# Kernel optimization log

Hardware: AMD Instinct MI355X
Metric: run time of the kernel (lower is better)

The kernel has to match this reference:

```python
import jax, jax.numpy as jnp
import numpy as np

H = 16        # attention heads
KVH = 4       # kv heads (GQA)
D = 128       # qk head_dim = qk_nope(64) + qk_rope(64)
ROPE = 64     # rotary sub-dim
VCH = 128     # v_channels
HID = 2048    # hidden size
E = 8         # routed experts
K = 2         # top-k
EPS = 1e-6
THETA = 10000.0


def rmsnorm(x, w):
    return x * jax.lax.rsqrt(jnp.mean(x * x, axis=-1, keepdims=True) + EPS) * w


def apply_rope(x, pos):
    # x: [T, h, ROPE]; rotate-half convention on the rope sub-dim
    half = ROPE // 2
    inv_freq = 1.0 / (THETA ** (jnp.arange(half, dtype=jnp.float32) / half))
    ang = pos.astype(jnp.float32)[:, None] * inv_freq          # [T, half]
    cos = jnp.cos(ang)[:, None, :]
    sin = jnp.sin(ang)[:, None, :]
    x1, x2 = x[..., :half], x[..., half:]
    return jnp.concatenate([x1 * cos - x2 * sin, x1 * sin + x2 * cos], axis=-1)


def swiglu(x, w_gate, w_up, w_down):
    return (jax.nn.silu(x @ w_gate) * (x @ w_up)) @ w_down


def setup_inputs() -> dict:
    key = jax.random.key(0)
    ks = jax.random.split(key, 16)
    T = 2048
    sc = 0.02
    n = lambda k, s: jax.random.normal(k, s, dtype=jnp.float32) * sc
    return {
        "x": jax.random.normal(ks[0], (T, HID), dtype=jnp.float32),
        "positions": jnp.arange(T, dtype=jnp.int32),
        "ln1_w": jnp.ones((HID,), jnp.float32),
        "qkv_w": n(ks[1], (HID, H * D + KVH * D + KVH * VCH)),
        "qkv_b": n(ks[2], (H * D + KVH * D + KVH * VCH,)),
        "k_ln_w": jnp.ones((D,), jnp.float32),
        "o_w": n(ks[3], (H * VCH, HID)),
        "ln2_w": jnp.ones((HID,), jnp.float32),
        "router_w": n(ks[4], (HID, E)),
        "w1": n(ks[5], (E, HID, 512)),
        "w2": n(ks[6], (E, 512, HID)),
        "w3": n(ks[7], (E, HID, 512)),
        "sw1": n(ks[8], (HID, 1024)),
        "sw2": n(ks[9], (1024, HID)),
        "sw3": n(ks[10], (HID, 1024)),
    }


def reference(x, positions, ln1_w, qkv_w, qkv_b, k_ln_w, o_w, ln2_w,
              router_w, w1, w2, w3, sw1, sw2, sw3):
    T = x.shape[0]
    # --- attention block ---
    h = rmsnorm(x, ln1_w)
    qkv = h @ qkv_w + qkv_b
    q = qkv[:, : H * D].reshape(T, H, D)
    k = qkv[:, H * D : H * D + KVH * D].reshape(T, KVH, D)
    v = qkv[:, H * D + KVH * D :].reshape(T, KVH, VCH)
    k = rmsnorm(k, k_ln_w)  # per-head k_layernorm over head_dim
    # rope applied to the trailing qk_rope_dim of q/k
    q = jnp.concatenate([q[..., : D - ROPE], apply_rope(q[..., D - ROPE :], positions)], -1)
    k = jnp.concatenate([k[..., : D - ROPE], apply_rope(k[..., D - ROPE :], positions)], -1)
    rep = H // KVH
    kf = jnp.repeat(k, rep, axis=1)   # [T, H, D]
    vf = jnp.repeat(v, rep, axis=1)   # [T, H, VCH]
    scale = D ** -0.5
    scores = jnp.einsum("qhd,khd->hqk", q, kf) * scale
    causal = jnp.tril(jnp.ones((T, T), dtype=bool))
    scores = jnp.where(causal[None], scores, jnp.float32(-1e30))
    p = jax.nn.softmax(scores, axis=-1)
    attn = jnp.einsum("hqk,khv->qhv", p, vf).reshape(T, H * VCH)
    x = x + attn @ o_w
    # --- MoE block: shared expert + top-k routed experts ---
    h2 = rmsnorm(x, ln2_w)
    probs = jax.nn.softmax(h2 @ router_w, axis=-1)            # [T, E]
    topw, topi = jax.lax.top_k(probs, K)
    topw = topw / jnp.sum(topw, axis=-1, keepdims=True)        # renormalize top-k
    combine = jnp.sum(jax.nn.one_hot(topi, E, dtype=h2.dtype) * topw[..., None], axis=1)  # [T, E]
    moe = swiglu(h2, sw1, sw3, sw2)                            # shared expert
    for e in range(E):  # small fixed expert count
        moe = moe + combine[:, e : e + 1] * swiglu(h2, w1[e], w3[e], w2[e])
    return x + moe
```

## Files before the change

### kernel.cpp

```cpp
#include <hip/hip_runtime.h>


typedef _Float16 half_t;
typedef _Float16 half8 __attribute__((ext_vector_type(8)));
typedef float    f32x4 __attribute__((ext_vector_type(4)));
typedef float    floatx4 __attribute__((ext_vector_type(4)));

#define T_TOK 2048
#define HIDN  2048
#define NH    16
#define NKVH  4
#define HD    128
#define QKV_N 3072
#define NEXP  8
#define NPAIR_MAX 4608

#define MFMA16(a,b,c) __builtin_amdgcn_mfma_f32_16x16x32_f16(a,b,c,0,0,0)

__device__ __forceinline__ void gload_lds16(const half_t* g, half_t* l) {
    __builtin_amdgcn_global_load_lds(
        (const __attribute__((address_space(1))) void*)g,
        (__attribute__((address_space(3))) void*)l, 16, 0, 0);
}

__device__ __forceinline__ float silu_f(float g) {
    return g / (1.0f + expf(-g));
}

__global__ __launch_bounds__(256)
void rmsnorm_split_k(const float* __restrict__ x, const float* __restrict__ w,
                     half_t* __restrict__ hi, half_t* __restrict__ lo)
{
    const int row = blockIdx.x, tid = threadIdx.x;
    const float* xr = x + (size_t)row * HIDN;
    floatx4 v0 = *(const floatx4*)(xr + tid * 8);
    floatx4 v1 = *(const floatx4*)(xr + tid * 8 + 4);
    float ss = v0[0]*v0[0] + v0[1]*v0[1] + v0[2]*v0[2] + v0[3]*v0[3]
             + v1[0]*v1[0] + v1[1]*v1[1] + v1[2]*v1[2] + v1[3]*v1[3];
    for (int o = 32; o; o >>= 1) ss += __shfl_down(ss, o);
    __shared__ float red[4];
    if ((tid & 63) == 0) red[tid >> 6] = ss;
    __syncthreads();
    ss = red[0] + red[1] + red[2] + red[3];
    float rs = rsqrtf(ss * (1.0f / HIDN) + 1e-6f);
    floatx4 w0 = *(const floatx4*)(w + tid * 8);
    floatx4 w1 = *(const floatx4*)(w + tid * 8 + 4);
    float vv[8] = { v0[0]*w0[0], v0[1]*w0[1], v0[2]*w0[2], v0[3]*w0[3],
                    v1[0]*w1[0], v1[1]*w1[1], v1[2]*w1[2], v1[3]*w1[3] };
    half8 hv, lv;
#pragma unroll
    for (int j = 0; j < 8; ++j) {
        float o = vv[j] * rs;
        half_t h = (half_t)o;
        hv[j] = h;
        lv[j] = (half_t)((o - (float)h) * 1024.0f);
    }
    *(half8*)(hi + (size_t)row * HIDN + tid * 8) = hv;
    if (lo) *(half8*)(lo + (size_t)row * HIDN + tid * 8) = lv;
}

__global__ __launch_bounds__(256)
void transpose_split2(const float* __restrict__ src,
                      half_t* __restrict__ dh, half_t* __restrict__ dl,
                      int sstride, int dstride)
{
    __shared__ float tile[32][36];
    const int n0 = blockIdx.x * 32, k0 = blockIdx.y * 32;
    const int tid = threadIdx.x;
    {
        int r = tid >> 3, c = (tid & 7) * 4;
        *(floatx4*)&tile[r][c] =
            *(const floatx4*)(src + (size_t)(k0 + r) * sstride + n0 + c);
    }
    __syncthreads();
    int n = tid & 31, g = tid >> 5, gg = g & 3;
    half8 hv;
    if (g < 4) {
#pragma unroll
        for (int j = 0; j < 8; ++j) hv[j] = (half_t)tile[gg * 8 + j][n];
        *(half8*)(dh + (size_t)(n0 + n) * dstride + k0 + gg * 8) = hv;
    } else {
#pragma unroll
        for (int j = 0; j < 8; ++j) {
            float v = tile[gg * 8 + j][n];
            half_t h = (half_t)v;
            hv[j] = (half_t)((v - (float)h) * 1024.0f);
        }
        *(half8*)(dl + (size_t)(n0 + n) * dstride + k0 + gg * 8) = hv;
    }
}

__global__ __launch_bounds__(256)
void transpose_f16(const float* __restrict__ src, half_t* __restrict__ dh,
                   int sstride, int dstride)
{
    __shared__ float tile[32][68];
    const int n0 = blockIdx.x * 64, k0 = blockIdx.y * 32;
    const int tid = threadIdx.x;
    {
        int r = tid >> 3, c = (tid & 7) * 4;
        const float* s = src + (size_t)(k0 + r) * sstride + n0;
        *(floatx4*)&tile[r][c]      = *(const floatx4*)(s + c);
        *(floatx4*)&tile[r][c + 32] = *(const floatx4*)(s + c + 32);
    }
    __syncthreads();
    int n = tid & 63, g = tid >> 6;
    half8 hv;
#pragma unroll
    for (int j = 0; j < 8; ++j) hv[j] = (half_t)tile[g * 8 + j][n];
    *(half8*)(dh + (size_t)(n0 + n) * dstride + k0 + g * 8) = hv;
}

__global__ __launch_bounds__(256)
void w13_transpose(const float* __restrict__ sw1, const float* __restrict__ w1,
                   const float* __restrict__ sw3, const float* __restrict__ w3,
                   half_t* __restrict__ dst)
{
    __shared__ float tile[32][68];
    const int n0 = blockIdx.x * 64, k0 = blockIdx.y * 32;
    const int tid = threadIdx.x;
    const float* base;
    int stride;
    if (n0 < 1024)      { base = sw1 + n0; stride = 1024; }
    else if (n0 < 2048) { base = sw3 + (n0 - 1024); stride = 1024; }
    else if (n0 < 6144) { int e = (n0 - 2048) >> 9;
                          base = w1 + (size_t)e * HIDN * 512 + ((n0 - 2048) & 511);
                          stride = 512; }
    else                { int e = (n0 - 6144) >> 9;
                          base = w3 + (size_t)e * HIDN * 512 + ((n0 - 6144) & 511);
                          stride = 512; }
    {
        int r = tid >> 3, c = (tid & 7) * 4;
        const float* s = base + (size_t)(k0 + r) * stride;
        *(floatx4*)&tile[r][c]      = *(const floatx4*)(s + c);
        *(floatx4*)&tile[r][c + 32] = *(const floatx4*)(s + c + 32);
    }
    __syncthreads();
    int n = tid & 63, g = tid >> 6;
    half8 hv;
#pragma unroll
    for (int j = 0; j < 8; ++j) hv[j] = (half_t)tile[g * 8 + j][n];
    *(half8*)(dst + (size_t)(n0 + n) * HIDN + k0 + g * 8) = hv;
}

__global__ __launch_bounds__(256)
void w2_transpose(const float* __restrict__ sw2, const float* __restrict__ w2,
                  half_t* __restrict__ dst)
{
    __shared__ float tile[32][68];
    const int n0 = blockIdx.x * 64, k0 = blockIdx.y * 32;
    const int tid = threadIdx.x;
    {
        int r = tid >> 3, c = (tid & 7) * 4;
        int k = k0 + r;
        const float* s;
        if (k < 1024) s = sw2 + (size_t)k * HIDN + n0;
        else {
            int e = (k - 1024) >> 9, kk = (k - 1024) & 511;
            s = w2 + ((size_t)e * 512 + kk) * HIDN + n0;
        }
        *(floatx4*)&tile[r][c]      = *(const floatx4*)(s + c);
        *(floatx4*)&tile[r][c + 32] = *(const floatx4*)(s + c + 32);
    }
    __syncthreads();
    int n = tid & 63, g = tid >> 6;
    half8 hv;
#pragma unroll
    for (int j = 0; j < 8; ++j) hv[j] = (half_t)tile[g * 8 + j][n];
    *(half8*)(dst + (size_t)(n0 + n) * 5120 + k0 + g * 8) = hv;
}

__global__ __launch_bounds__(256)
void owu_kernel(const float* __restrict__ ow, const float* __restrict__ ln2w,
                const float* __restrict__ rw, float* __restrict__ owu,
                int* __restrict__ cnt, int* __restrict__ pairTok,
                float* __restrict__ pairW)
{
    if (blockIdx.x < 18) {
        int idx = blockIdx.x * 256 + threadIdx.x;
        if (idx < NPAIR_MAX) { pairTok[idx] = 0; pairW[idx] = 0.0f; }
        if (idx < NEXP) cnt[idx] = 0;
    }
    const int k = blockIdx.x * 4 + (threadIdx.x >> 6);
    const int lane = threadIdx.x & 63;
    float acc[NEXP] = {};
    const float* row = ow + (size_t)k * HIDN;
#pragma unroll
    for (int j = 0; j < 8; ++j) {
        int c = j * 256 + lane * 4;
        floatx4 ov = *(const floatx4*)(row + c);
        floatx4 lw = *(const floatx4*)(ln2w + c);
#pragma unroll
        for (int i = 0; i < 4; ++i) {
            float s = ov[i] * lw[i];
            const float* rwc = rw + (size_t)(c + i) * NEXP;
#pragma unroll
            for (int e = 0; e < NEXP; ++e) acc[e] += s * rwc[e];
        }
    }
#pragma unroll
    for (int e = 0; e < NEXP; ++e)
        for (int o = 32; o; o >>= 1) acc[e] += __shfl_down(acc[e], o);
    if (lane == 0) {
#pragma unroll
        for (int e = 0; e < NEXP; ++e) owu[(size_t)k * NEXP + e] = acc[e];
    }
}

template<bool SPLIT, int BM>
__global__ __launch_bounds__(256, 2)
void gemm_f16(const half_t* __restrict__ Ah, const half_t* __restrict__ Al,
              const half_t* __restrict__ Bth, const half_t* __restrict__ Btl,
              const float* __restrict__ bias, const float* __restrict__ res,
              float* __restrict__ Cf, half_t* __restrict__ Ch,
              int M, int N, int K, int lda, int ldb)
{
    constexpr int NBUF = SPLIT ? 2 : 1;
    constexpr int MR = BM / 32;
    __shared__ half_t As[2][NBUF][BM * 32];
    __shared__ half_t Bs[2][NBUF][128 * 32];
    const int tid = threadIdx.x, lane = tid & 63, wid = tid >> 6;
    const int l15 = lane & 15, l4 = lane >> 4;
    const int row0 = blockIdx.y * BM, col0 = blockIdx.x * 128;
    const int wr = (wid >> 1) * (BM / 2), wc = (wid & 1) * 64;
    f32x4 accM[MR][4] = {}, accC[MR][4] = {};
    const int lrw = lane >> 2, lcl = (lane & 3) * 8;

#define STAGE(BUF, K0)                                                        \
    do {                                                                      \
        _Pragma("unroll")                                                     \
        for (int j = 0; j < BM / 64; ++j) {                                   \
            const int r = wid * (BM / 4) + j * 16;                            \
            const size_t ga = (size_t)(row0 + r + lrw) * lda + (K0) + lcl;    \
            gload_lds16(Ah + ga, &As[BUF][0][r * 32]);                        \
            if constexpr (SPLIT) gload_lds16(Al + ga, &As[BUF][1][r * 32]);   \
        }                                                                     \
        _Pragma("unroll")                                                     \
        for (int j = 0; j < 2; ++j) {                                         \
            const int r = wid * 32 + j * 16;                                  \
            const size_t gb = (size_t)(col0 + r + lrw) * ldb + (K0) + lcl;    \
            gload_lds16(Bth + gb, &Bs[BUF][0][r * 32]);                       \
            if constexpr (SPLIT) gload_lds16(Btl + gb, &Bs[BUF][1][r * 32]);  \
        }                                                                     \
    } while (0)

    STAGE(0, 0);
    __syncthreads();
    int cur = 0;
    for (int k0 = 0; k0 < K; k0 += 32, cur ^= 1) {
        if (k0 + 32 < K) STAGE(cur ^ 1, k0 + 32);
        half8 ah[MR], al[MR], bh[4], bl[4];
#pragma unroll
        for (int m = 0; m < MR; ++m) {
            int off = (wr + m * 16 + l15) * 32 + l4 * 8;
            ah[m] = *(const half8*)&As[cur][0][off];
            if constexpr (SPLIT) al[m] = *(const half8*)&As[cur][1][off];
        }
#pragma unroll
        for (int n = 0; n < 4; ++n) {
            int off = (wc + n * 16 + l15) * 32 + l4 * 8;
            bh[n] = *(const half8*)&Bs[cur][0][off];
            if constexpr (SPLIT) bl[n] = *(const half8*)&Bs[cur][1][off];
        }
#pragma unroll
        for (int m = 0; m < MR; ++m)
#pragma unroll
            for (int n = 0; n < 4; ++n) {
                accM[m][n] = MFMA16(ah[m], bh[n], accM[m][n]);
                if constexpr (SPLIT) {
                    accC[m][n] = MFMA16(ah[m], bl[n], accC[m][n]);
                    accC[m][n] = MFMA16(al[m], bh[n], accC[m][n]);
                }
            }
        __syncthreads();
    }
#undef STAGE

#pragma unroll
    for (int m = 0; m < MR; ++m) {
#pragma unroll
        for (int n = 0; n < 4; ++n) {
            int gr0 = row0 + wr + m * 16 + l4 * 4;
            int gc  = col0 + wc + n * 16 + l15;
            float b = bias ? bias[gc] : 0.0f;
#pragma unroll
            for (int i = 0; i < 4; ++i) {
                float v = accM[m][n][i];
                if constexpr (SPLIT) v += accC[m][n][i] * (1.0f / 1024.0f);
                v += b;
                size_t idx = (size_t)(gr0 + i) * N + gc;
                if (res) v += res[idx];
                if (Cf) Cf[idx] = v;
                if (Ch) Ch[idx] = (half_t)v;
            }
        }
    }
}

template<bool GROUPED>
__global__ __launch_bounds__(256, 2)
void gemm_gu_act(const half_t* __restrict__ h2, const half_t* __restrict__ W13t,
                 const int* __restrict__ pairTok, const int* __restrict__ basep,
                 const float* __restrict__ pairW, half_t* __restrict__ outp)
{
    __shared__ half_t As[2][64 * 32];
    __shared__ half_t Bs[2][128 * 32];
    __shared__ half_t ex[64][136];
    const int tid = threadIdx.x, lane = tid & 63, wid = tid >> 6;
    const int l15 = lane & 15, l4 = lane >> 4;
    const int lrw = lane >> 2, lcl = (lane & 3) * 8;
    const int ct = blockIdx.x, row0 = blockIdx.y * 64;
    int gbase, ubase;
    if constexpr (GROUPED) {
        int e = 0;
#pragma unroll
        for (int i = 1; i < NEXP; ++i) if (row0 >= basep[i]) e = i;
        gbase = 2048 + 512 * e + ct * 64;
        ubase = 6144 + 512 * e + ct * 64;
    } else {
        gbase = ct * 64;
        ubase = 1024 + ct * 64;
    }
    const int wr = (wid >> 1) * 32, wc = (wid & 1) * 64;
    const half_t* Abase;
    if constexpr (GROUPED) {
        const int tok = pairTok[row0 + wid * 16 + lrw];
        Abase = h2 + (size_t)tok * HIDN + lcl;
    } else {
        Abase = h2 + (size_t)(row0 + wid * 16 + lrw) * HIDN + lcl;
    }
    f32x4 acc[2][4] = {};

#define GSTAGE(BUF, K0)                                                       \
    do {                                                                      \
        gload_lds16(Abase + (K0), &As[BUF][(wid * 16) * 32]);                 \
        _Pragma("unroll")                                                     \
        for (int j = 0; j < 2; ++j) {                                         \
            const int r = wid * 32 + j * 16;                                  \
            const int grow = (r < 64) ? gbase + r : ubase + (r - 64);         \
            const size_t gb = (size_t)(grow + lrw) * HIDN + (K0) + lcl;       \
            gload_lds16(W13t + gb, &Bs[BUF][r * 32]);                         \
        }                                                                     \
    } while (0)

    GSTAGE(0, 0);
    __syncthreads();
    int cur = 0;
    for (int k0 = 0; k0 < HIDN; k0 += 32, cur ^= 1) {
        if (k0 + 32 < HIDN) GSTAGE(cur ^ 1, k0 + 32);
        half8 ah[2], bh[4];
#pragma unroll
        for (int m = 0; m < 2; ++m)
            ah[m] = *(const half8*)&As[cur][(wr + m * 16 + l15) * 32 + l4 * 8];
#pragma unroll
        for (int n = 0; n < 4; ++n)
            bh[n] = *(const half8*)&Bs[cur][(wc + n * 16 + l15) * 32 + l4 * 8];
#pragma unroll
        for (int m = 0; m < 2; ++m)
// ... 33 lines not shown
void gemm_down_all(const half_t* __restrict__ As_sh, const half_t* __restrict__ Ab,
                   const half_t* __restrict__ W2t, const int* __restrict__ basep,
                   const float* __restrict__ x2, float* __restrict__ out,
                   half_t* __restrict__ Ypair)
{
    __shared__ half_t Asm[2][64 * 32];
    __shared__ half_t Bsm[2][128 * 32];
    const int tid = threadIdx.x, lane = tid & 63, wid = tid >> 6;
    const int l15 = lane & 15, l4 = lane >> 4;
    const int lrw = lane >> 2, lcl = (lane & 3) * 8;
    const int col0 = blockIdx.x * 128;
    const bool shared = (blockIdx.y < 32);
    const int row0 = (shared ? blockIdx.y : blockIdx.y - 32) * 64;
    const half_t* A;
    int lda, K, bcol;
    if (shared) { A = As_sh; lda = 1024; K = 1024; bcol = 0; }
    else {
        int e = 0;
#pragma unroll
        for (int i = 1; i < NEXP; ++i) if (row0 >= basep[i]) e = i;
        A = Ab; lda = 512; K = 512; bcol = 1024 + 512 * e;
    }
    const int wr = (wid >> 1) * 32, wc = (wid & 1) * 64;
    f32x4 acc[2][4] = {};

#define DSTAGE(BUF, K0)                                                       \
    do {                                                                      \
        const size_t ga = (size_t)(row0 + wid * 16 + lrw) * lda + (K0) + lcl; \
        gload_lds16(A + ga, &Asm[BUF][(wid * 16) * 32]);                      \
        _Pragma("unroll")                                                     \
        for (int j = 0; j < 2; ++j) {                                         \
            const int r = wid * 32 + j * 16;                                  \
            const size_t gb = (size_t)(col0 + r + lrw) * 5120 + bcol + (K0) + lcl; \
            gload_lds16(W2t + gb, &Bsm[BUF][r * 32]);                         \
        }                                                                     \
    } while (0)

    DSTAGE(0, 0);
    __syncthreads();
    int cur = 0;
    for (int k0 = 0; k0 < K; k0 += 32, cur ^= 1) {
        if (k0 + 32 < K) DSTAGE(cur ^ 1, k0 + 32);
        half8 ah[2], bh[4];
#pragma unroll
        for (int m = 0; m < 2; ++m)
            ah[m] = *(const half8*)&Asm[cur][(wr + m * 16 + l15) * 32 + l4 * 8];
#pragma unroll
        for (int n = 0; n < 4; ++n)
            bh[n] = *(const half8*)&Bsm[cur][(wc + n * 16 + l15) * 32 + l4 * 8];
#pragma unroll
        for (int m = 0; m < 2; ++m)
#pragma unroll
            for (int n = 0; n < 4; ++n)
                acc[m][n] = MFMA16(ah[m], bh[n], acc[m][n]);
        __syncthreads();
    }
#undef DSTAGE

#pragma unroll
    for (int m = 0; m < 2; ++m)
#pragma unroll
        for (int n = 0; n < 4; ++n) {
            int gr0 = row0 + wr + m * 16 + l4 * 4;
            int gc  = col0 + wc + n * 16 + l15;
#pragma unroll
            for (int i = 0; i < 4; ++i) {
                size_t idx = (size_t)(gr0 + i) * HIDN + gc;
                if (shared) out[idx] = x2[idx] + acc[m][n][i];
                else        Ypair[idx] = (half_t)acc[m][n][i];
            }
        }
}

__global__ __launch_bounds__(256)
void qkv_prep(const float* __restrict__ qkv, const int* __restrict__ pos,
              const float* __restrict__ klnw,
              half_t* __restrict__ qh, half_t* __restrict__ ql,
              half_t* __restrict__ kh, half_t* __restrict__ kl)
{
    const int t = blockIdx.x, tid = threadIdx.x, lane = tid & 63, wid = tid >> 6;
    const float* row = qkv + (size_t)t * QKV_N;
    __shared__ float cs[32], sn[32];
    if (tid < 32) {
        double freq = exp((double)tid * -0.28782313662425572);
        double ang = (double)pos[t] * freq;
        const double twopi = 6.283185307179586476925286766559;
        ang -= twopi * floor(ang * (1.0 / twopi));
        float a = (float)ang;
        cs[tid] = cosf(a);
        sn[tid] = sinf(a);
    }
    __syncthreads();

    const float qscale = 0.08838834764831845f;
    {
        const int hh = tid >> 4, d0 = (tid & 15) * 8;
        const float* qrow = row + hh * HD;
        float outv[8];
        if (d0 < 64) {
#pragma unroll
            for (int j = 0; j < 8; ++j) outv[j] = qrow[d0 + j];
        } else if (d0 < 96) {
            int j0 = d0 - 64;
#pragma unroll
            for (int j = 0; j < 8; ++j) {
                int jj = j0 + j;
                outv[j] = qrow[64 + jj] * cs[jj] - qrow[96 + jj] * sn[jj];
            }
        } else {
            int j0 = d0 - 96;
#pragma unroll
            for (int j = 0; j < 8; ++j) {
                int jj = j0 + j;
                outv[j] = qrow[64 + jj] * sn[jj] + qrow[96 + jj] * cs[jj];
            }
        }
        half8 hv, lv;
#pragma unroll
        for (int j = 0; j < 8; ++j) {
            float o = outv[j] * qscale;
            half_t h = (half_t)o;
            hv[j] = h;
            lv[j] = (half_t)((o - (float)h) * 1024.0f);
        }
        size_t base = (size_t)t * (NH * HD) + hh * HD + d0;
        *(half8*)(qh + base) = hv;
        *(half8*)(ql + base) = lv;
    }
    {
        const float* krow = row + NH * HD + wid * HD;
        float a0 = krow[lane], a1 = krow[64 + lane];
        float ss = a0 * a0 + a1 * a1;
        for (int o = 32; o; o >>= 1) ss += __shfl_down(ss, o);
        ss = __shfl(ss, 0);
        float rs = rsqrtf(ss * (1.0f / HD) + 1e-6f);
        float n0 = a0 * rs * klnw[lane];
        float n1 = a1 * rs * klnw[64 + lane];
        float other = __shfl_xor(n1, 32);
        int j = lane & 31;
        float o1 = (lane < 32) ? (n1 * cs[j] - other * sn[j])
                               : (other * sn[j] + n1 * cs[j]);
        size_t base = (size_t)t * (NKVH * HD) + wid * HD;
        half_t h;
        h = (half_t)n0; kh[base + lane] = h;
        kl[base + lane] = (half_t)((n0 - (float)h) * 1024.0f);
        h = (half_t)o1; kh[base + 64 + lane] = h;
        kl[base + 64 + lane] = (half_t)((o1 - (float)h) * 1024.0f);
    }
}

__global__ __launch_bounds__(256, 2)
void attn_kernel(const half_t* __restrict__ qh, const half_t* __restrict__ ql,
                 const half_t* __restrict__ kh, const half_t* __restrict__ kl,
                 const half_t* __restrict__ vth, const half_t* __restrict__ vtl,
                 half_t* __restrict__ oh, half_t* __restrict__ ol,
                 float* __restrict__ Op0, float* __restrict__ Op1,
                 float* __restrict__ Op2, float* __restrict__ ml)
{
    const int bid = blockIdx.x;
    const int h = bid & 15;
    int rrem = bid >> 4, q = 31, nch = 6, c = 0;
    for (; q >= 0; --q) {
        nch = (q + 6) / 6;
        if (rrem < nch) { c = rrem; break; }
        rrem -= nch;
    }
    const int nt = 2 * (q + 1);
    const int kvbeg = ((c * nt) / nch) * 32;
    const int kvend = (((c + 1) * nt) / nch) * 32;

    const int kvh = h >> 2;
    const int tid = threadIdx.x, lane = tid & 63, wid = tid >> 6;
    const int q0 = q * 64 + wid * 16;
    const int l15 = lane & 15, l4 = lane >> 4;

    __shared__ half_t Ksh[32][136], Ksl[32][136];
    __shared__ half_t Vsh[128][40], Vsl[128][40];
    __shared__ half_t Ph[4][16][40], Pl[4][16][40];

    half8 qfh[4], qfl[4];
    {
        const size_t qb = (size_t)(q0 + l15) * (NH * HD) + h * HD + l4 * 8;
#pragma unroll
        for (int cc = 0; cc < 4; ++cc) {
            qfh[cc] = *(const half8*)(qh + qb + cc * 32);
            qfl[cc] = *(const half8*)(ql + qb + cc * 32);
        }
    }

    f32x4 om[8] = {}, oc[8] = {};
    float mrow[4] = { -1e30f, -1e30f, -1e30f, -1e30f };
    float lrow[4] = {};

    const int kr = tid >> 4, kc = (tid & 15) * 8;
    const int vd = tid >> 2, vc = (tid & 3) * 8;
    uint4 rk0h, rk1h, rk0l, rk1l, rv0h, rv1h, rv0l, rv1l;

#define LOAD_TILE(KV0)                                                        \
    do {                                                                      \
        size_t sk0 = (size_t)((KV0) + kr) * (NKVH * HD) + kvh * HD + kc;      \
        size_t sk1 = sk0 + (size_t)16 * (NKVH * HD);                          \
        rk0h = *(const uint4*)(kh + sk0);  rk0l = *(const uint4*)(kl + sk0);  \
        rk1h = *(const uint4*)(kh + sk1);  rk1l = *(const uint4*)(kl + sk1);  \
        size_t sv0 = (size_t)(kvh * HD + vd) * T_TOK + (KV0) + vc;            \
        size_t sv1 = sv0 + (size_t)64 * T_TOK;                                \
        rv0h = *(const uint4*)(vth + sv0); rv0l = *(const uint4*)(vtl + sv0); \
        rv1h = *(const uint4*)(vth + sv1); rv1l = *(const uint4*)(vtl + sv1); \
    } while (0)

    LOAD_TILE(kvbeg);
    for (int kv0 = kvbeg; kv0 < kvend; kv0 += 32) {
        *(uint4*)&Ksh[kr][kc]      = rk0h;  *(uint4*)&Ksl[kr][kc]      = rk0l;
        *(uint4*)&Ksh[kr + 16][kc] = rk1h;  *(uint4*)&Ksl[kr + 16][kc] = rk1l;
        *(uint4*)&Vsh[vd][vc]      = rv0h;  *(uint4*)&Vsl[vd][vc]      = rv0l;
        *(uint4*)&Vsh[vd + 64][vc] = rv1h;  *(uint4*)&Vsl[vd + 64][vc] = rv1l;
        __syncthreads();
        if (kv0 + 32 < kvend) LOAD_TILE(kv0 + 32);

        f32x4 sf[2];
        __builtin_amdgcn_s_setprio(1);
#pragma unroll
        for (int t2 = 0; t2 < 2; ++t2) {
            f32x4 s = {}, sc = {};
#pragma unroll
            for (int cc = 0; cc < 4; ++cc) {
                half8 bh = *(const half8*)&Ksh[t2 * 16 + l15][cc * 32 + l4 * 8];
                half8 bl = *(const half8*)&Ksl[t2 * 16 + l15][cc * 32 + l4 * 8];
                s  = MFMA16(qfh[cc], bh, s);
                sc = MFMA16(qfh[cc], bl, sc);
                sc = MFMA16(qfl[cc], bh, sc);
            }
            sf[t2] = s + sc * (1.0f / 1024.0f);
        }
        __builtin_amdgcn_s_setprio(0);

        float pmax[4];
#pragma unroll
        for (int i = 0; i < 4; ++i) {
            const int qg = q0 + l4 * 4 + i;
#pragma unroll
            for (int t2 = 0; t2 < 2; ++t2) {
                int kvg = kv0 + t2 * 16 + l15;
                if (kvg > qg) sf[t2][i] = -1e30f;
            }
            float mx = fmaxf(sf[0][i], sf[1][i]);
#pragma unroll
            for (int o = 1; o < 16; o <<= 1) mx = fmaxf(mx, __shfl_xor(mx, o));
            pmax[i] = mx;
        }
        float dm = fmaxf(fmaxf(pmax[0] - mrow[0], pmax[1] - mrow[1]),
                         fmaxf(pmax[2] - mrow[2], pmax[3] - mrow[3]));
        if (__any(dm > 6.0f)) {
#pragma unroll
            for (int i = 0; i < 4; ++i) {
                float mnew = fmaxf(mrow[i], pmax[i]);
                float resc = expf(mrow[i] - mnew);
                lrow[i] *= resc;
#pragma unroll
                for (int c8 = 0; c8 < 8; ++c8) {
                    om[c8][i] *= resc; oc[c8][i] *= resc;
                }
                mrow[i] = mnew;
            }
        }
#pragma unroll
        for (int i = 0; i < 4; ++i) {
            float p0 = expf(sf[0][i] - mrow[i]);
            float p1 = expf(sf[1][i] - mrow[i]);
            lrow[i] += p0 + p1;
            half_t hh;
            hh = (half_t)p0;
            Ph[wid][l4 * 4 + i][l15] = hh;
            Pl[wid][l4 * 4 + i][l15] = (half_t)((p0 - (float)hh) * 1024.0f);
            hh = (half_t)p1;
            Ph[wid][l4 * 4 + i][16 + l15] = hh;
            Pl[wid][l4 * 4 + i][16 + l15] = (half_t)((p1 - (float)hh) * 1024.0f);
        }

        half8 pah = *(const half8*)&Ph[wid][l15][l4 * 8];
        half8 pal = *(const half8*)&Pl[wid][l15][l4 * 8];
        __builtin_amdgcn_s_setprio(1);
#pragma unroll
        for (int c8 = 0; c8 < 8; ++c8) {
            half8 vh = *(const half8*)&Vsh[c8 * 16 + l15][l4 * 8];
            half8 vl = *(const half8*)&Vsl[c8 * 16 + l15][l4 * 8];
            om[c8] = MFMA16(pah, vh, om[c8]);
            oc[c8] = MFMA16(pah, vl, oc[c8]);
            oc[c8] = MFMA16(pal, vh, oc[c8]);
        }
        __builtin_amdgcn_s_setprio(0);
        __syncthreads();
    }
#undef LOAD_TILE

#pragma unroll
    for (int i = 0; i < 4; ++i)
#pragma unroll
        for (int o = 1; o < 16; o <<= 1) lrow[i] += __shfl_xor(lrow[i], o);

    if (nch == 1) {
#pragma unroll
        for (int c8 = 0; c8 < 8; ++c8) {
#pragma unroll
            for (int i = 0; i < 4; ++i) {
                float v = (om[c8][i] + oc[c8][i] * (1.0f / 1024.0f)) / lrow[i];
                size_t idx = (size_t)(q0 + l4 * 4 + i) * (NH * HD) + h * HD
                           + c8 * 16 + l15;
                half_t hh = (half_t)v;
                oh[idx] = hh;
                ol[idx] = (half_t)((v - (float)hh) * 1024.0f);
            }
        }
    } else {
        float* Op = (bid < 768)  ? Op0 + (size_t)bid * 8192
                  : (bid < 1280) ? Op1 + (size_t)(bid - 768) * 8192
                                 : Op2 + (size_t)(bid - 1280) * 8192;
#pragma unroll
        for (int c8 = 0; c8 < 8; ++c8) {
#pragma unroll
            for (int i = 0; i < 4; ++i) {
                int row64 = wid * 16 + l4 * 4 + i;
                Op[row64 * 128 + c8 * 16 + l15] =
                    om[c8][i] + oc[c8][i] * (1.0f / 1024.0f);
            }
        }
        if (l15 == 0) {
#pragma unroll
            for (int i = 0; i < 4; ++i) {
                int row64 = wid * 16 + l4 * 4 + i;
                ml[(size_t)bid * 128 + row64]      = mrow[i];
                ml[(size_t)bid * 128 + 64 + row64] = lrow[i];
            }
        }
    }
}

__device__ __forceinline__ const float* slot_ptr(int s, const float* Op0,
                                                 const float* Op1,
                                                 const float* Op2)
{
    return (s < 768)  ? Op0 + (size_t)s * 8192
         : (s < 1280) ? Op1 + (size_t)(s - 768) * 8192
                      : Op2 + (size_t)(s - 1280) * 8192;
}

__global__ __launch_bounds__(256)
void attn_combine(const float* __restrict__ Op0, const float* __restrict__ Op1,
                  const float* __restrict__ Op2, const float* __restrict__ ml,
                  half_t* __restrict__ oh, half_t* __restrict__ ol)
{
    const int bid = blockIdx.x;
    const int h = bid & 15, q = 6 + (bid >> 4);
    const int nch = (q + 6) / 6;
    int r0 = 0;
    for (int j = 31; j > q; --j) r0 += (j + 6) / 6;
    const int tid = threadIdx.x;
    const int row = tid >> 2, cg = (tid & 3) * 32;

    float M = -1e30f;
    for (int c = 0; c < nch; ++c) {
        int s = (r0 + c) * 16 + h;
        M = fmaxf(M, ml[(size_t)s * 128 + row]);
    }
    float wsum = 0.0f;
    for (int c = 0; c < nch; ++c) {
        int s = (r0 + c) * 16 + h;
        wsum += ml[(size_t)s * 128 + 64 + row] *
                expf(ml[(size_t)s * 128 + row] - M);
    }
    float inv = 1.0f / wsum;

    size_t obase = (size_t)(q * 64 + row) * (NH * HD) + h * HD + cg;
#pragma unroll
    for (int jj = 0; jj < 4; ++jj) {
        floatx4 a0 = {0,0,0,0}, a1 = {0,0,0,0};
        for (int c = 0; c < nch; ++c) {
            int s = (r0 + c) * 16 + h;
            float w = expf(ml[(size_t)s * 128 + row] - M) * inv;
            const float* base = slot_ptr(s, Op0, Op1, Op2) + row * 128 + cg;
            a0 += w * (*(const floatx4*)(base + jj * 8));
            a1 += w * (*(const floatx4*)(base + jj * 8 + 4));
        }
        half8 hv, lvv;
#pragma unroll
        for (int k = 0; k < 4; ++k) {
            half_t hh = (half_t)a0[k];
            hv[k] = hh; lvv[k] = (half_t)((a0[k] - (float)hh) * 1024.0f);
            hh = (half_t)a1[k];
            hv[4 + k] = hh; lvv[4 + k] = (half_t)((a1[k] - (float)hh) * 1024.0f);
        }
        *(half8*)(oh + obase + jj * 8) = hv;
        *(half8*)(ol + obase + jj * 8) = lvv;
    }
}

__global__ __launch_bounds__(256)
void router_linear(const float* __restrict__ x, const half_t* __restrict__ ah,
                   const half_t* __restrict__ al, const float* __restrict__ x2,
                   const float* __restrict__ ln2w, const float* __restrict__ rw,
                   const float* __restrict__ owu,
                   int* __restrict__ topi, float* __restrict__ topv,
                   int* __restrict__ cnt, half_t* __restrict__ h2)
{
    const int t = blockIdx.x, tid = threadIdx.x;
    const float* xr2 = x2 + (size_t)t * HIDN + tid * 8;
    floatx4 x2a = *(const floatx4*)(xr2);
    floatx4 x2b = *(const floatx4*)(xr2 + 4);
    float ss = x2a[0]*x2a[0] + x2a[1]*x2a[1] + x2a[2]*x2a[2] + x2a[3]*x2a[3]
             + x2b[0]*x2b[0] + x2b[1]*x2b[1] + x2b[2]*x2b[2] + x2b[3]*x2b[3];
    for (int o = 32; o; o >>= 1) ss += __shfl_down(ss, o);
    __shared__ float red[4];
    if ((tid & 63) == 0) red[tid >> 6] = ss;
    __syncthreads();
    ss = red[0] + red[1] + red[2] + red[3];
    float rs = rsqrtf(ss * (1.0f / HIDN) + 1e-6f);

    const float* xr = x + (size_t)t * HIDN + tid * 8;
    floatx4 xa = *(const floatx4*)(xr);
    floatx4 xb = *(const floatx4*)(xr + 4);
    floatx4 lwa = *(const floatx4*)(ln2w + tid * 8);
    floatx4 lwb = *(const floatx4*)(ln2w + tid * 8 + 4);
    half8 av  = *(const half8*)(ah + (size_t)t * HIDN + tid * 8);
    half8 alv = *(const half8*)(al + (size_t)t * HIDN + tid * 8);

    float acc[NEXP] = {};
#pragma unroll
    for (int j = 0; j < 8; ++j) {
        int c = tid * 8 + j;
        float xv = (j < 4 ? xa[j] : xb[j - 4]) * (j < 4 ? lwa[j] : lwb[j - 4]);
        float ap = (float)av[j] + (float)alv[j] * (1.0f / 1024.0f);
        const float* rwc = rw + (size_t)c * NEXP;
        const float* owc = owu + (size_t)c * NEXP;
#pragma unroll
        for (int e = 0; e < NEXP; ++e) acc[e] += xv * rwc[e] + ap * owc[e];
    }
#pragma unroll
    for (int e = 0; e < NEXP; ++e)
        for (int o = 32; o; o >>= 1) acc[e] += __shfl_down(acc[e], o);
    __shared__ float red8[4][NEXP];
    if ((tid & 63) == 0)
#pragma unroll
        for (int e = 0; e < NEXP; ++e) red8[tid >> 6][e] = acc[e];

    half8 h2v;
#pragma unroll
    for (int j = 0; j < 8; ++j) {
        float xv = (j < 4 ? x2a[j] : x2b[j - 4]) * (j < 4 ? lwa[j] : lwb[j - 4]);
        h2v[j] = (half_t)(xv * rs);
    }
    *(half8*)(h2 + (size_t)t * HIDN + tid * 8) = h2v;

    __syncthreads();
    if (tid == 0) {
        float lg[NEXP];
#pragma unroll
        for (int e = 0; e < NEXP; ++e)
            lg[e] = (red8[0][e] + red8[1][e] + red8[2][e] + red8[3][e]) * rs;
        int i1 = 0;
        for (int e = 1; e < NEXP; ++e) if (lg[e] > lg[i1]) i1 = e;
        int i2 = (i1 == 0) ? 1 : 0;
        for (int e = 0; e < NEXP; ++e) if (e != i1 && lg[e] > lg[i2]) i2 = e;
        float mx = lg[i1];
        float p1 = expf(lg[i1] - mx), p2 = expf(lg[i2] - mx);
        float inv = 1.0f / (p1 + p2);
        topi[2 * t] = i1;       topi[2 * t + 1] = i2;
        topv[2 * t] = p1 * inv; topv[2 * t + 1] = p2 * inv;
        atomicAdd(&cnt[i1], 1);
        atomicAdd(&cnt[i2], 1);
    }
}

__global__ __launch_bounds__(256)
void moe_build(const int* __restrict__ cnt, int* __restrict__ basep,
               const int* __restrict__ topi, const float* __restrict__ topv,
               int* __restrict__ pairTok, float* __restrict__ pairW,
               int* __restrict__ pairPos)
{
    const int e = blockIdx.x;
    int base = 0;
    for (int i = 0; i < e; ++i) base += (cnt[i] + 63) & ~63;
    if (threadIdx.x == 0) basep[e] = base;

    const int tid = threadIdx.x, lane = tid & 63, wv = tid >> 6;
    __shared__ int wsum[4];
    int run = base;
    for (int i0 = 0; i0 < 2 * T_TOK; i0 += 256) {
        int i = i0 + tid;
        bool m = (topi[i] == e);
        unsigned long long bal = __ballot(m);
        int lpre = __popcll(bal & ((1ull << lane) - 1ull));
        if (lane == 0) wsum[wv] = (int)__popcll(bal);
        __syncthreads();
        int woff = 0;
        for (int w = 0; w < wv; ++w) woff += wsum[w];
        if (m) {
            int pos = run + woff + lpre;
            pairTok[pos] = i >> 1;
            pairW[pos]   = topv[i];
            pairPos[i]   = pos;
        }
        run += wsum[0] + wsum[1] + wsum[2] + wsum[3];
        __syncthreads();
    }
}

__global__ __launch_bounds__(256)
void moe_final(const half_t* __restrict__ Ypair, const int* __restrict__ pairPos,
               float* __restrict__ out)
{
    int t = blockIdx.x, c0 = threadIdx.x * 8;
    int p1 = pairPos[2 * t], p2 = pairPos[2 * t + 1];
    half8 y1 = *(const half8*)(Ypair + (size_t)p1 * HIDN + c0);
    half8 y2 = *(const half8*)(Ypair + (size_t)p2 * HIDN + c0);
    float* o = out + (size_t)t * HIDN + c0;
    floatx4 a = *(floatx4*)o, b = *(floatx4*)(o + 4);
#pragma unroll
    for (int j = 0; j < 4; ++j) {
        a[j] += (float)y1[j] + (float)y2[j];
        b[j] += (float)y1[4 + j] + (float)y2[4 + j];
    }
    *(floatx4*)o = a;
    *(floatx4*)(o + 4) = b;
}

extern "C" void kernel_launch(void* const* d_in, const int* in_sizes, int n_in,
                              void* d_out, int out_size, void* d_ws, size_t ws_size,
                              hipStream_t stream)
{
    (void)in_sizes; (void)n_in; (void)out_size; (void)ws_size;
    const float* x    = (const float*)d_in[0];
    const int*   pos  = (const int*)  d_in[1];
    const float* ln1w = (const float*)d_in[2];
    const float* qkvw = (const float*)d_in[3];
    const float* qkvb = (const float*)d_in[4];
    const float* klnw = (const float*)d_in[5];
    const float* ow   = (const float*)d_in[6];
    const float* ln2w = (const float*)d_in[7];
    const float* rw   = (const float*)d_in[8];
    const float* w1   = (const float*)d_in[9];
    const float* w2   = (const float*)d_in[10];
    const float* w3   = (const float*)d_in[11];
    const float* sw1  = (const float*)d_in[12];
    const float* sw2  = (const float*)d_in[13];
    const float* sw3  = (const float*)d_in[14];
    float* out = (float*)d_out;

    char* ws = (char*)d_ws;
    const size_t AB = 16842752;
    float*  x2      = (float*)(ws);
    half_t* h_hi    = (half_t*)(ws + AB);
    half_t* h_lo    = (half_t*)(ws + AB + 8388608);
    half_t* qkvwt_h = (half_t*)(ws + AB + 16777216);
    half_t* qkvwt_l = (half_t*)(ws + AB + 29360128);
    float*  qkv     = (float*)(ws + AB + 41943040);
    half_t* q_h     = (half_t*)(ws + AB + 67108864);
    half_t* q_l     = (half_t*)(ws + AB + 75497472);
    half_t* k_h     = (half_t*)(ws + AB + 83886080);
    half_t* k_l     = (half_t*)(ws + AB + 85983232);
    half_t* vt_h    = (half_t*)(ws + AB + 88080384);
    half_t* vt_l    = (half_t*)(ws + AB + 90177536);
    half_t* attn_h  = (half_t*)(ws + AB);
    half_t* attn_l  = (half_t*)(ws + AB + 8388608);
    half_t* owt     = (half_t*)(ws + AB + 16777216);
    float*  ow_u    = (float*)(ws + AB + 25165824);
    float*  mlpart  = (float*)(ws + AB + 25231360);
    float*  Opart0  = (float*)(ws + AB + 41943040);
    float*  Opart1  = (float*)(ws);
    float*  Opart2  = (float*)(ws + AB + 29360128);
    half_t* h2      = (half_t*)(ws + AB + 33554432);
    half_t* W13t    = (half_t*)(ws + AB + 41943040);
    half_t* As_sh   = (half_t*)(ws + AB);
    half_t* Ab      = (half_t*)(ws + AB + 16777216);
    half_t* W2t     = (half_t*)(ws + AB + 41943040);
    half_t* Ypair   = (half_t*)(ws + AB + 92274688);

    char* meta = ws + (size_t)(AB + 117440512);
    int*    cnt     = (int*)  (meta + 0);
    int*    basep   = (int*)  (meta + 128);
    int*    topi    = (int*)  (meta + 256);
    float*  topv    = (float*)(meta + 16640);
    int*    pairPos = (int*)  (meta + 33024);
    int*    pairTok = (int*)  (meta + 49408);
    float*  pairW   = (float*)(meta + 67840);

    dim3 b256(256);

    rmsnorm_split_k<<<T_TOK, b256, 0, stream>>>(x, ln1w, h_hi, h_lo);
    transpose_split2<<<dim3(QKV_N / 32, HIDN / 32), b256, 0, stream>>>(
        qkvw, qkvwt_h, qkvwt_l, QKV_N, HIDN);
    gemm_f16<true, 64><<<dim3(QKV_N / 128, T_TOK / 64), b256, 0, stream>>>(
        h_hi, h_lo, qkvwt_h, qkvwt_l, qkvb, nullptr, qkv, nullptr,
        T_TOK, QKV_N, HIDN, HIDN, HIDN);
    qkv_prep<<<T_TOK, b256, 0, stream>>>(qkv, pos, klnw, q_h, q_l, k_h, k_l);
    transpose_split2<<<dim3(512 / 32, T_TOK / 32), b256, 0, stream>>>(
        qkv + 2560, vt_h, vt_l, QKV_N, T_TOK);
    transpose_f16<<<dim3(HIDN / 64, HIDN / 32), b256, 0, stream>>>(
        ow, owt, HIDN, HIDN);
    owu_kernel<<<512, b256, 0, stream>>>(ow, ln2w, rw, ow_u,
                                         cnt, pairTok, pairW);
    attn_kernel<<<1632, b256, 0, stream>>>(
        q_h, q_l, k_h, k_l, vt_h, vt_l, attn_h, attn_l,
        Opart0, Opart1, Opart2, mlpart);
    attn_combine<<<416, b256, 0, stream>>>(Opart0, Opart1, Opart2, mlpart,
                                           attn_h, attn_l);
    gemm_f16<false, 64><<<dim3(HIDN / 128, T_TOK / 64), b256, 0, stream>>>(
        attn_h, nullptr, owt, nullptr, nullptr, x, x2, nullptr,
        T_TOK, HIDN, HIDN, HIDN, HIDN);
    router_linear<<<T_TOK, b256, 0, stream>>>(
        x, attn_h, attn_l, x2, ln2w, rw, ow_u, topi, topv, cnt, h2);
    moe_build<<<NEXP, b256, 0, stream>>>(cnt, basep, topi, topv,
                                         pairTok, pairW, pairPos);
    w13_transpose<<<dim3(10240 / 64, HIDN / 32), b256, 0, stream>>>(
        sw1, w1, sw3, w3, W13t);
    gemm_gu_act<false><<<dim3(16, T_TOK / 64), b256, 0, stream>>>(
        h2, W13t, nullptr, nullptr, nullptr, As_sh);
    gemm_gu_act<true><<<dim3(8, NPAIR_MAX / 64), b256, 0, stream>>>(
        h2, W13t, pairTok, basep, pairW, Ab);
    w2_transpose<<<dim3(HIDN / 64, 5120 / 32), b256, 0, stream>>>(sw2, w2, W2t);
    gemm_down_all<<<dim3(16, 104), b256, 0, stream>>>(
        As_sh, Ab, W2t, basep, x2, out, Ypair);
    moe_final<<<T_TOK, b256, 0, stream>>>(Ypair, pairPos, out);
}
```

Measured before the change: 629.8 us.

## Route logits via per-head V·owu projections; drop low-half split precision in P·V

Router logits previously depended on the attention output in split hi/lo precision. Now each V row is projected onto the router directions (owu) up front in a new z_kernel. These 8-wide per-head values are carried through the attention softmax in fp32 and combined across chunks, so the router gets full-precision contributions without the low-half attention output. This drops the Vsl/Pl buffers and two thirds of the P·V MFMAs, plus the vt_l and attn_l stores. It adds a small extra kernel, extra shuffles and partial buffers, and leaves the attention output in single fp16.

```diff
diff --git a/kernel.cpp b/kernel.cpp
--- a/kernel.cpp
+++ b/kernel.cpp
@@ -3,6 +3,7 @@
 
 typedef _Float16 half_t;
 typedef _Float16 half8 __attribute__((ext_vector_type(8)));
+typedef _Float16 half2v __attribute__((ext_vector_type(2)));
 typedef float    f32x4 __attribute__((ext_vector_type(4)));
 typedef float    floatx4 __attribute__((ext_vector_type(4)));
 
@@ -109,6 +110,29 @@
 #pragma unroll
     for (int j = 0; j < 8; ++j) hv[j] = (half_t)tile[g * 8 + j][n];
     *(half8*)(dh + (size_t)(n0 + n) * dstride + k0 + g * 8) = hv;
+}
+
+__global__ __launch_bounds__(256)
+void vt_transpose_perm(const float* __restrict__ src, half_t* __restrict__ dh)
+{
+    __shared__ float tile[32][68];
+    const int n0 = blockIdx.x * 64, k0 = blockIdx.y * 32;
+    const int tid = threadIdx.x;
+    {
+        int r = tid >> 3, c = (tid & 7) * 4;
+        const float* s = src + (size_t)(k0 + r) * QKV_N + n0;
+        *(floatx4*)&tile[r][c]      = *(const floatx4*)(s + c);
+        *(floatx4*)&tile[r][c + 32] = *(const floatx4*)(s + c + 32);
+    }
+    __syncthreads();
+    int n = tid & 63, g = tid >> 6;
+    half8 hv;
+#pragma unroll
+    for (int tt = 0; tt < 8; ++tt) {
+        int c_src = (tt & 1) * 16 + 4 * g + (tt >> 1);
+        hv[tt] = (half_t)tile[c_src][n];
+    }
+    *(half8*)(dh + (size_t)(n0 + n) * T_TOK + k0 + g * 8) = hv;
 }
 
 __global__ __launch_bounds__(256)
@@ -204,6 +228,32 @@
     if (lane == 0) {
 #pragma unroll
         for (int e = 0; e < NEXP; ++e) owu[(size_t)k * NEXP + e] = acc[e];
+    }
+}
+
+__global__ __launch_bounds__(256)
+void z_kernel(const float* __restrict__ qkv, const float* __restrict__ owu,
+              float* __restrict__ zbuf)
+{
+    const int kv = blockIdx.x, tid = threadIdx.x;
+    const int hh = tid >> 4, li = tid & 15;
+    const float* vrow = qkv + (size_t)kv * QKV_N + 2560 + (hh >> 2) * HD;
+    const int d0 = li * 8;
+    float acc[NEXP] = {};
+#pragma unroll
+    for (int j = 0; j < 8; ++j) {
+        float v = vrow[d0 + j];
+        const float* ou = owu + (size_t)(hh * HD + d0 + j) * NEXP;
+#pragma unroll
+        for (int e = 0; e < NEXP; ++e) acc[e] += v * ou[e];
+    }
+#pragma unroll
+    for (int e = 0; e < NEXP; ++e)
+        for (int o = 1; o < 16; o <<= 1) acc[e] += __shfl_xor(acc[e], o);
+    if (li == 0) {
+#pragma unroll
+        for (int e = 0; e < NEXP; ++e)
+            zbuf[((size_t)hh * T_TOK + kv) * NEXP + e] = acc[e];
     }
 }
 
@@ -543,10 +593,11 @@
 __global__ __launch_bounds__(256, 2)
 void attn_kernel(const half_t* __restrict__ qh, const half_t* __restrict__ ql,
                  const half_t* __restrict__ kh, const half_t* __restrict__ kl,
-                 const half_t* __restrict__ vth, const half_t* __restrict__ vtl,
-                 half_t* __restrict__ oh, half_t* __restrict__ ol,
+                 const half_t* __restrict__ vth, const float* __restrict__ zbuf,
+                 half_t* __restrict__ oh,
                  float* __restrict__ Op0, float* __restrict__ Op1,
-                 float* __restrict__ Op2, float* __restrict__ ml)
+                 float* __restrict__ Op2, float* __restrict__ ml,
+                 float* __restrict__ zpart, float* __restrict__ zfin)
 {
     const int bid = blockIdx.x;
     const int h = bid & 15;
@@ -566,8 +617,9 @@
     const int l15 = lane & 15, l4 = lane >> 4;
 
     __shared__ half_t Ksh[32][136], Ksl[32][136];
-    __shared__ half_t Vsh[128][40], Vsl[128][40];
-    __shared__ half_t Ph[4][16][40], Pl[4][16][40];
+    __shared__ half_t Vsh[128][40];
+    __shared__ half_t Ph[4][16][40];
+    __shared__ float  zsh[32][8];
 
     half8 qfh[4], qfl[4];
     {
@@ -579,13 +631,16 @@
         }
     }
 
-    f32x4 om[8] = {}, oc[8] = {};
+    f32x4 om[8] = {};
+    f32x4 zacA[4] = {}, zacB[4] = {};
     float mrow[4] = { -1e30f, -1e30f, -1e30f, -1e30f };
     float lrow[4] = {};
 
     const int kr = tid >> 4, kc = (tid & 15) * 8;
     const int vd = tid >> 2, vc = (tid & 3) * 8;
-    uint4 rk0h, rk1h, rk0l, rk1l, rv0h, rv1h, rv0l, rv1l;
+    const int zrr = tid >> 3, zrc = tid & 7;
+    uint4 rk0h, rk1h, rk0l, rk1l, rv0h, rv1h;
+    float rz;
 
 #define LOAD_TILE(KV0)                                                        \
     do {                                                                      \
@@ -595,16 +650,18 @@
         rk1h = *(const uint4*)(kh + sk1);  rk1l = *(const uint4*)(kl + sk1);  \
         size_t sv0 = (size_t)(kvh * HD + vd) * T_TOK + (KV0) + vc;            \
         size_t sv1 = sv0 + (size_t)64 * T_TOK;                                \
-        rv0h = *(const uint4*)(vth + sv0); rv0l = *(const uint4*)(vtl + sv0); \
-        rv1h = *(const uint4*)(vth + sv1); rv1l = *(const uint4*)(vtl + sv1); \
+        rv0h = *(const uint4*)(vth + sv0);                                    \
+        rv1h = *(const uint4*)(vth + sv1);                                    \
+        rz = zbuf[((size_t)h * T_TOK + (KV0) + zrr) * 8 + zrc];               \
     } while (0)
 
     LOAD_TILE(kvbeg);
     for (int kv0 = kvbeg; kv0 < kvend; kv0 += 32) {
         *(uint4*)&Ksh[kr][kc]      = rk0h;  *(uint4*)&Ksl[kr][kc]      = rk0l;
         *(uint4*)&Ksh[kr + 16][kc] = rk1h;  *(uint4*)&Ksl[kr + 16][kc] = rk1l;
-        *(uint4*)&Vsh[vd][vc]      = rv0h;  *(uint4*)&Vsl[vd][vc]      = rv0l;
-        *(uint4*)&Vsh[vd + 64][vc] = rv1h;  *(uint4*)&Vsl[vd + 64][vc] = rv1l;
+        *(uint4*)&Vsh[vd][vc]      = rv0h;
+        *(uint4*)&Vsh[vd + 64][vc] = rv1h;
+        zsh[zrr][zrc] = rz;
         __syncthreads();
         if (kv0 + 32 < kvend) LOAD_TILE(kv0 + 32);
 
@@ -612,16 +669,16 @@
         __builtin_amdgcn_s_setprio(1);
 #pragma unroll
         for (int t2 = 0; t2 < 2; ++t2) {
-            f32x4 s = {}, sc = {};
+            f32x4 s = {}, sc1 = {}, sc2 = {};
 #pragma unroll
             for (int cc = 0; cc < 4; ++cc) {
                 half8 bh = *(const half8*)&Ksh[t2 * 16 + l15][cc * 32 + l4 * 8];
                 half8 bl = *(const half8*)&Ksl[t2 * 16 + l15][cc * 32 + l4 * 8];
-                s  = MFMA16(qfh[cc], bh, s);
-                sc = MFMA16(qfh[cc], bl, sc);
-                sc = MFMA16(qfl[cc], bh, sc);
-            }
-            sf[t2] = s + sc * (1.0f / 1024.0f);
+                s   = MFMA16(qfh[cc], bh, s);
+                sc1 = MFMA16(qfh[cc], bl, sc1);
+                sc2 = MFMA16(qfl[cc], bh, sc2);
+            }
+            sf[t2] = s + (sc1 + sc2) * (1.0f / 1024.0f);
         }
         __builtin_amdgcn_s_setprio(0);
 
@@ -647,37 +704,33 @@
                 float mnew = fmaxf(mrow[i], pmax[i]);
                 float resc = expf(mrow[i] - mnew);
                 lrow[i] *= resc;
-#pragma unroll
-                for (int c8 = 0; c8 < 8; ++c8) {
-                    om[c8][i] *= resc; oc[c8][i] *= resc;
-                }
+                zacA[i] *= resc;  zacB[i] *= resc;
+#pragma unroll
+                for (int c8 = 0; c8 < 8; ++c8) om[c8][i] *= resc;
                 mrow[i] = mnew;
             }
         }
+        f32x4 za0 = *(const f32x4*)&zsh[l15][0];
+        f32x4 za1 = *(const f32x4*)&zsh[l15][4];
+        f32x4 zb0 = *(const f32x4*)&zsh[16 + l15][0];
+        f32x4 zb1 = *(const f32x4*)&zsh[16 + l15][4];
 #pragma unroll
         for (int i = 0; i < 4; ++i) {
             float p0 = expf(sf[0][i] - mrow[i]);
             float p1 = expf(sf[1][i] - mrow[i]);
             lrow[i] += p0 + p1;
-            half_t hh;
-            hh = (half_t)p0;
-            Ph[wid][l4 * 4 + i][l15] = hh;
-            Pl[wid][l4 * 4 + i][l15] = (half_t)((p0 - (float)hh) * 1024.0f);
-            hh = (half_t)p1;
-            Ph[wid][l4 * 4 + i][16 + l15] = hh;
-            Pl[wid][l4 * 4 + i][16 + l15] = (half_t)((p1 - (float)hh) * 1024.0f);
+            zacA[i] += p0 * za0 + p1 * zb0;
+            zacB[i] += p0 * za1 + p1 * zb1;
+            half2v pp = { (half_t)p0, (half_t)p1 };
+            *(half2v*)&Ph[wid][l4 * 4 + i][l15 * 2] = pp;
         }
 
         half8 pah = *(const half8*)&Ph[wid][l15][l4 * 8];
-        half8 pal = *(const half8*)&Pl[wid][l15][l4 * 8];
         __builtin_amdgcn_s_setprio(1);
 #pragma unroll
         for (int c8 = 0; c8 < 8; ++c8) {
             half8 vh = *(const half8*)&Vsh[c8 * 16 + l15][l4 * 8];
-            half8 vl = *(const half8*)&Vsl[c8 * 16 + l15][l4 * 8];
             om[c8] = MFMA16(pah, vh, om[c8]);
-            oc[c8] = MFMA16(pah, vl, oc[c8]);
-            oc[c8] = MFMA16(pal, vh, oc[c8]);
         }
         __builtin_amdgcn_s_setprio(0);
         __syncthreads();
@@ -689,17 +742,41 @@
 #pragma unroll
         for (int o = 1; o < 16; o <<= 1) lrow[i] += __shfl_xor(lrow[i], o);
 
+    for (int o = 1; o < 16; o <<= 1) {
+#pragma unroll
+        for (int i = 0; i < 4; ++i)
+#pragma unroll
+            for (int k = 0; k < 4; ++k) {
+                zacA[i][k] += __shfl_xor(zacA[i][k], o);
+                zacB[i][k] += __shfl_xor(zacB[i][k], o);
+            }
+    }
+    if (l15 == 0) {
+#pragma unroll
+        for (int i = 0; i < 4; ++i) {
+            int row64 = wid * 16 + l4 * 4 + i;
+            if (nch == 1) {
+                float invl = 1.0f / lrow[i];
+                size_t zo = ((size_t)(q * 64 + row64) * 16 + h) * 8;
+                *(f32x4*)&zfin[zo]     = zacA[i] * invl;
+                *(f32x4*)&zfin[zo + 4] = zacB[i] * invl;
+            } else {
+                size_t zo = ((size_t)bid * 64 + row64) * 8;
+                *(f32x4*)&zpart[zo]     = zacA[i];
+                *(f32x4*)&zpart[zo + 4] = zacB[i];
+            }
+        }
+    }
+
     if (nch == 1) {
 #pragma unroll
         for (int c8 = 0; c8 < 8; ++c8) {
 #pragma unroll
             for (int i = 0; i < 4; ++i) {
-                float v = (om[c8][i] + oc[c8][i] * (1.0f / 1024.0f)) / lrow[i];
+                float v = om[c8][i] / lrow[i];
                 size_t idx = (size_t)(q0 + l4 * 4 + i) * (NH * HD) + h * HD
                            + c8 * 16 + l15;
-                half_t hh = (half_t)v;
-                oh[idx] = hh;
-                ol[idx] = (half_t)((v - (float)hh) * 1024.0f);
+                oh[idx] = (half_t)v;
             }
         }
     } else {
@@ -711,8 +788,7 @@
 #pragma unroll
             for (int i = 0; i < 4; ++i) {
                 int row64 = wid * 16 + l4 * 4 + i;
-                Op[row64 * 128 + c8 * 16 + l15] =
-                    om[c8][i] + oc[c8][i] * (1.0f / 1024.0f);
+                Op[row64 * 128 + c8 * 16 + l15] = om[c8][i];
             }
         }
         if (l15 == 0) {
@@ -738,7 +814,8 @@
 __global__ __launch_bounds__(256)
 void attn_combine(const float* __restrict__ Op0, const float* __restrict__ Op1,
                   const float* __restrict__ Op2, const float* __restrict__ ml,
-                  half_t* __restrict__ oh, half_t* __restrict__ ol)
+                  const float* __restrict__ zpart,
+                  half_t* __restrict__ oh, float* __restrict__ zfin)
 {
     const int bid = blockIdx.x;
     const int h = bid & 15, q = 6 + (bid >> 4);
@@ -760,6 +837,20 @@
                 expf(ml[(size_t)s * 128 + row] - M);
     }
     float inv = 1.0f / wsum;
+
+    if ((tid & 3) == 0) {
+        f32x4 a = {0,0,0,0}, b = {0,0,0,0};
+        for (int c = 0; c < nch; ++c) {
+            int s = (r0 + c) * 16 + h;
+            float w = expf(ml[(size_t)s * 128 + row] - M) * inv;
+            size_t zo = ((size_t)s * 64 + row) * 8;
+            a += w * (*(const f32x4*)&zpart[zo]);
+            b += w * (*(const f32x4*)&zpart[zo + 4]);
+        }
+        size_t zo = ((size_t)(q * 64 + row) * 16 + h) * 8;
+        *(f32x4*)&zfin[zo]     = a;
+        *(f32x4*)&zfin[zo + 4] = b;
+    }
 
     size_t obase = (size_t)(q * 64 + row) * (NH * HD) + h * HD + cg;
 #pragma unroll
@@ -772,24 +863,20 @@
             a0 += w * (*(const floatx4*)(base + jj * 8));
             a1 += w * (*(const floatx4*)(base + jj * 8 + 4));
         }
-        half8 hv, lvv;
+        half8 hv;
 #pragma unroll
         for (int k = 0; k < 4; ++k) {
-            half_t hh = (half_t)a0[k];
-            hv[k] = hh; lvv[k] = (half_t)((a0[k] - (float)hh) * 1024.0f);
-            hh = (half_t)a1[k];
-            hv[4 + k] = hh; lvv[4 + k] = (half_t)((a1[k] - (float)hh) * 1024.0f);
+            hv[k]     = (half_t)a0[k];
+            hv[4 + k] = (half_t)a1[k];
         }
         *(half8*)(oh + obase + jj * 8) = hv;
-        *(half8*)(ol + obase + jj * 8) = lvv;
-    }
-}
-
-__global__ __launch_bounds__(256)
-void router_linear(const float* __restrict__ x, const half_t* __restrict__ ah,
-                   const half_t* __restrict__ al, const float* __restrict__ x2,
+    }
+}
+
+__global__ __launch_bounds__(256)
+void router_linear(const float* __restrict__ x, const float* __restrict__ zfin,
+                   const float* __restrict__ x2,
                    const float* __restrict__ ln2w, const float* __restrict__ rw,
-                   const float* __restrict__ owu,
                    int* __restrict__ topi, float* __restrict__ topv,
                    int* __restrict__ cnt, half_t* __restrict__ h2)
 {
@@ -811,19 +898,15 @@
     floatx4 xb = *(const floatx4*)(xr + 4);
     floatx4 lwa = *(const floatx4*)(ln2w + tid * 8);
     floatx4 lwb = *(const floatx4*)(ln2w + tid * 8 + 4);
-    half8 av  = *(const half8*)(ah + (size_t)t * HIDN + tid * 8);
-    half8 alv = *(const half8*)(al + (size_t)t * HIDN + tid * 8);
 
     float acc[NEXP] = {};
 #pragma unroll
     for (int j = 0; j < 8; ++j) {
         int c = tid * 8 + j;
         float xv = (j < 4 ? xa[j] : xb[j - 4]) * (j < 4 ? lwa[j] : lwb[j - 4]);
-        float ap = (float)av[j] + (float)alv[j] * (1.0f / 1024.0f);
         const float* rwc = rw + (size_t)c * NEXP;
-        const float* owc = owu + (size_t)c * NEXP;
-#pragma unroll
-        for (int e = 0; e < NEXP; ++e) acc[e] += xv * rwc[e] + ap * owc[e];
+#pragma unroll
+        for (int e = 0; e < NEXP; ++e) acc[e] += xv * rwc[e];
     }
 #pragma unroll
     for (int e = 0; e < NEXP; ++e)
@@ -833,6 +916,12 @@
 #pragma unroll
         for (int e = 0; e < NEXP; ++e) red8[tid >> 6][e] = acc[e];
 
+    __shared__ float zred[NEXP * 16];
+    if (tid < 128) {
+        int hh = tid >> 3, e = tid & 7;
+        zred[e * 16 + hh] = zfin[((size_t)t * 16 + hh) * 8 + e];
+    }
+
     half8 h2v;
 #pragma unroll
     for (int j = 0; j < 8; ++j) {
@@ -845,8 +934,12 @@
     if (tid == 0) {
         float lg[NEXP];
 #pragma unroll
-        for (int e = 0; e < NEXP; ++e)
-            lg[e] = (red8[0][e] + red8[1][e] + red8[2][e] + red8[3][e]) * rs;
+        for (int e = 0; e < NEXP; ++e) {
+            float zs = 0.0f;
+#pragma unroll
+            for (int hh = 0; hh < 16; ++hh) zs += zred[e * 16 + hh];
+            lg[e] = (red8[0][e] + red8[1][e] + red8[2][e] + red8[3][e] + zs) * rs;
+        }
         int i1 = 0;
         for (int e = 1; e < NEXP; ++e) if (lg[e] > lg[i1]) i1 = e;
         int i2 = (i1 == 0) ? 1 : 0;
@@ -949,9 +1042,8 @@
     half_t* k_h     = (half_t*)(ws + AB + 83886080);
     half_t* k_l     = (half_t*)(ws + AB + 85983232);
     half_t* vt_h    = (half_t*)(ws + AB + 88080384);
-    half_t* vt_l    = (half_t*)(ws + AB + 90177536);
     half_t* attn_h  = (half_t*)(ws + AB);
-    half_t* attn_l  = (half_t*)(ws + AB + 8388608);
+    float*  zbuf    = (float*)(ws + AB + 8388608);
     half_t* owt     = (half_t*)(ws + AB + 16777216);
     float*  ow_u    = (float*)(ws + AB + 25165824);
     float*  mlpart  = (float*)(ws + AB + 25231360);
@@ -973,6 +1065,8 @@
     int*    pairPos = (int*)  (meta + 33024);
     int*    pairTok = (int*)  (meta + 49408);
     float*  pairW   = (float*)(meta + 67840);
+    float*  zpart   = (float*)(meta + 131072);
+    float*  zfin    = (float*)(meta + 131072 + 3342336);
 
     dim3 b256(256);
 
@@ -983,22 +1077,23 @@
         h_hi, h_lo, qkvwt_h, qkvwt_l, qkvb, nullptr, qkv, nullptr,
         T_TOK, QKV_N, HIDN, HIDN, HIDN);
     qkv_prep<<<T_TOK, b256, 0, stream>>>(qkv, pos, klnw, q_h, q_l, k_h, k_l);
-    transpose_split2<<<dim3(512 / 32, T_TOK / 32), b256, 0, stream>>>(
-        qkv + 2560, vt_h, vt_l, QKV_N, T_TOK);
+    vt_transpose_perm<<<dim3(512 / 64, T_TOK / 32), b256, 0, stream>>>(
+        qkv + 2560, vt_h);
     transpose_f16<<<dim3(HIDN / 64, HIDN / 32), b256, 0, stream>>>(
         ow, owt, HIDN, HIDN);
     owu_kernel<<<512, b256, 0, stream>>>(ow, ln2w, rw, ow_u,
                                          cnt, pairTok, pairW);
+    z_kernel<<<T_TOK, b256, 0, stream>>>(qkv, ow_u, zbuf);
     attn_kernel<<<1632, b256, 0, stream>>>(
-        q_h, q_l, k_h, k_l, vt_h, vt_l, attn_h, attn_l,
-        Opart0, Opart1, Opart2, mlpart);
+        q_h, q_l, k_h, k_l, vt_h, zbuf, attn_h,
+        Opart0, Opart1, Opart2, mlpart, zpart, zfin);
     attn_combine<<<416, b256, 0, stream>>>(Opart0, Opart1, Opart2, mlpart,
-                                           attn_h, attn_l);
+                                           zpart, attn_h, zfin);
     gemm_f16<false, 64><<<dim3(HIDN / 128, T_TOK / 64), b256, 0, stream>>>(
         attn_h, nullptr, owt, nullptr, nullptr, x, x2, nullptr,
         T_TOK, HIDN, HIDN, HIDN, HIDN);
     router_linear<<<T_TOK, b256, 0, stream>>>(
-        x, attn_h, attn_l, x2, ln2w, rw, ow_u, topi, topv, cnt, h2);
+        x, zfin, x2, ln2w, rw, topi, topv, cnt, h2);
     moe_build<<<NEXP, b256, 0, stream>>>(cnt, basep, topi, topv,
                                          pairTok, pairW, pairPos);
     w13_transpose<<<dim3(10240 / 64, HIDN / 32), b256, 0, stream>>>(
```

New measurement: 621.1 us. No clear change (-1.4%).
